# Kernel tuning notes

Measured on AMD Instinct MI355X. Metric: run time of the kernel, lower is better.

The kernel has to match this reference:

```python
import jax, jax.numpy as jnp
import numpy as np

N = 100000      # nodes
E = 800000      # edges
IN1 = 128       # gcn input feature dim
IN2 = 64        # lstm input feature dim
H = 128         # hidden_channels
B = 32          # lstm batch
T = 200         # lstm seq len
OUT = 1         # out_channels
TARGET = jnp.array([0, 1000, 2000, 3000, 4000, 5000, 6000, 7000])  # numgcnE=8


def setup_inputs() -> dict:
    key = jax.random.key(0)
    ks = jax.random.split(key, 20)
    s = 0.05
    inp = {
        "data0": jax.random.normal(ks[0], (B, T, IN2), jnp.float32),
        "data1": jax.random.normal(ks[1], (N, IN1), jnp.float32),
        "edge_index": jax.random.randint(ks[2], (2, E), 0, N, dtype=jnp.int64),
        # GCNConv layers (weight stored [in, out])
        "W1": jax.random.normal(ks[3], (IN1, H), jnp.float32) * s,
        "b1": jnp.zeros((H,), jnp.float32),
        "W2": jax.random.normal(ks[4], (H, H), jnp.float32) * s,
        "b2": jnp.zeros((H,), jnp.float32),
        # LSTM1 (gate order i,f,g,o as in torch)
        "Wih1": jax.random.normal(ks[5], (4 * H, IN2), jnp.float32) * s,
        "Whh1": jax.random.normal(ks[6], (4 * H, H), jnp.float32) * s,
        "bih1": jnp.zeros((4 * H,), jnp.float32),
        "bhh1": jnp.zeros((4 * H,), jnp.float32),
        # LSTM2
        "Wih2": jax.random.normal(ks[7], (4 * H, H), jnp.float32) * s,
        "Whh2": jax.random.normal(ks[8], (4 * H, H), jnp.float32) * s,
        "bih2": jnp.zeros((4 * H,), jnp.float32),
        "bhh2": jnp.zeros((4 * H,), jnp.float32),
        # MLP head: (numgcnE+1)*H -> (numgcnE+1)*H/2 -> OUT
        "m1_w": jax.random.normal(ks[9], (9 * H, 9 * H // 2), jnp.float32) * s,
        "m1_b": jnp.zeros((9 * H // 2,), jnp.float32),
        "m2_w": jax.random.normal(ks[10], (9 * H // 2, OUT), jnp.float32) * s,
        "m2_b": jnp.zeros((OUT,), jnp.float32),
    }
    return inp


def gcn_conv(x, W, b, src, dst, n):
    # PyG GCNConv: self-loops + symmetric normalization, then scatter-add.
    xw = x @ W                                                     # [N, H]
    ones = jnp.ones(src.shape[0], xw.dtype)
    deg = jax.ops.segment_sum(ones, dst, num_segments=n) + 1.0     # +1 self-loop
    dinv = jax.lax.rsqrt(deg)                                      # [N]
    norm = dinv[src] * dinv[dst]                                   # [E]
    agg = jax.ops.segment_sum(xw[src] * norm[:, None], dst, num_segments=n)
    agg = agg + xw * (dinv * dinv)[:, None]                        # self-loop msgs
    return agg + b


def lstm_final(x_tbi, Wih, Whh, bih, bhh):
    # x_tbi: [T, Bsz, in]; returns final hidden state h_T [Bsz, H]
    Bsz = x_tbi.shape[1]
    Hh = Whh.shape[1]
    bias = bih + bhh

    def step(carry, xt):
        h, c = carry
        g = xt @ Wih.T + h @ Whh.T + bias                          # [Bsz, 4H]
        i, f, gg, o = jnp.split(g, 4, axis=-1)
        c = jax.nn.sigmoid(f) * c + jax.nn.sigmoid(i) * jnp.tanh(gg)
        h = jax.nn.sigmoid(o) * jnp.tanh(c)
        return (h, c), None

    init = (jnp.zeros((Bsz, Hh), x_tbi.dtype), jnp.zeros((Bsz, Hh), x_tbi.dtype))
    (h, c), _ = jax.lax.scan(step, init, x_tbi)
    return h


def reference(data0, data1, edge_index, W1, b1, W2, b2,
              Wih1, Whh1, bih1, bhh1, Wih2, Whh2, bih2, bhh2,
              m1_w, m1_b, m2_w, m2_b):
    src, dst = edge_index[0], edge_index[1]
    n = data1.shape[0]
    # two GCN layers with ReLU
    h = jax.nn.relu(gcn_conv(data1, W1, b1, src, dst, n))
    h = jax.nn.relu(gcn_conv(h, W2, b2, src, dst, n))
    g = h[TARGET].reshape(-1)                                      # [numgcnE*H]
    # lstm1 over [B, T, IN2] (batch_first) -> final h_n [B, H]
    h1 = lstm_final(jnp.swapaxes(data0, 0, 1), Wih1, Whh1, bih1, bhh1)
    # lstm2 consumes h_n[None] as [batch=1, seq=B, H] -> final h [1, H]
    h2 = lstm_final(h1[:, None, :], Wih2, Whh2, bih2, bhh2)[0]     # [H]
    d = jnp.concatenate([g, h2])                                   # [(numgcnE+1)*H]
    return (d @ m1_w + m1_b) @ m2_w + m2_b                         # [OUT]
```

## Files before the change

### kernel.cpp

```cpp
#include <hip/hip_runtime.h>
#include <hip/hip_bf16.h>
#include <cstring>

using bf16 = __hip_bfloat16;
typedef _Float16 h2v __attribute__((ext_vector_type(2)));
typedef _Float16 h8v __attribute__((ext_vector_type(8)));

#if __has_builtin(__builtin_amdgcn_fdot2)
__device__ __forceinline__ float FDOT2(h2v a, h2v b, float c) {
    return __builtin_amdgcn_fdot2(a, b, c, false);
}
#else
__device__ __forceinline__ float FDOT2(h2v a, h2v b, float c) {
    return c + (float)a.x * (float)b.x + (float)a.y * (float)b.y;
}
#endif

__device__ __forceinline__ float sigm_f(float x) {
    return __builtin_amdgcn_rcpf(1.f + __expf(-x));
}
__device__ __forceinline__ float tanh_f(float x) {
    return 1.f - 2.f * __builtin_amdgcn_rcpf(1.f + __expf(2.f * x));
}

constexpr int NH    = 128;
constexpr int G4    = 512;
constexpr int TSEQ  = 200;
constexpr int BBATCH= 32;
constexpr int NTGT  = 8;

constexpr int LCAP1 = 1024;
constexpr int S1CAP = LCAP1 + NTGT;
constexpr int LCAP2 = 8192;
constexpr int S2CAP = LCAP2 + S1CAP;

constexpr size_t algn(size_t x) { return (x + 255) & ~size_t(255); }
constexpr size_t OFF_GX1  = 0;
constexpr size_t OFF_GX2  = algn(OFF_GX1  + 6400ull * G4 * 4);
constexpr size_t OFF_DEG  = algn(OFF_GX2  + 32ull * G4 * 4);
constexpr size_t OFF_DINV = algn(OFF_DEG  + 100000ull * 4);
constexpr size_t OFF_SL1  = algn(OFF_DINV + 100000ull * 4);
constexpr size_t OFF_SL2  = algn(OFF_SL1  + 100000ull * 4);
constexpr size_t OFF_CNT  = algn(OFF_SL2  + 100000ull * 4);
constexpr size_t OFF_L1   = algn(OFF_CNT  + 64);
constexpr size_t OFF_S1   = algn(OFF_L1   + (size_t)LCAP1 * 8);
constexpr size_t OFF_L2   = algn(OFF_S1   + (size_t)S1CAP * 4);
constexpr size_t OFF_S2   = algn(OFF_L2   + (size_t)LCAP2 * 8);
constexpr size_t OFF_XW1  = algn(OFF_S2   + (size_t)S2CAP * 4);
constexpr size_t OFF_H1   = algn(OFF_XW1  + (size_t)S2CAP * NH * 4);
constexpr size_t OFF_XW2  = algn(OFF_H1   + (size_t)S1CAP * NH * 4);
constexpr size_t OFF_DVEC = algn(OFF_XW2  + (size_t)S1CAP * NH * 4);
constexpr size_t OFF_H1F  = algn(OFF_DVEC + 1152ull * 4);
constexpr size_t OFF_CACC = algn(OFF_H1F  + 32ull * NH * 4);
constexpr size_t WS_NEEDED = OFF_CACC + 576ull * 4;

__device__ __forceinline__ int edge_at(const int* ei, int E, int is64, int row, int e) {
    return is64 ? ei[(((size_t)row * E) + e) * 2] : ei[((size_t)row * E) + e];
}

__device__ __forceinline__ float dinv_of(const int* deg, int v) {
    return rsqrtf((float)deg[v] + 1.0f);
}

__global__ void k_canary(unsigned int* out, unsigned int bits) {
    if (threadIdx.x == 0) out[0] = bits;
}


__global__ void k_init(const int* ei, int* deg, int* slot1, int* slot2, int* cnt,
                       float* colacc, int n) {
    int i = blockIdx.x * 256 + threadIdx.x;
    if (i < 14) cnt[i] = 0;
    if (i == 15) cnt[15] = (ei[1] == 0 && ei[3] == 0 && ei[5] == 0 && ei[7] == 0) ? 1 : 0;
    if (i < 576) colacc[i] = 0.f;
    for (; i < n; i += gridDim.x * 256) { deg[i] = 0; slot1[i] = -1; slot2[i] = -1; }
}

__global__ void k_deg_l1(const int* ei, int E, int* deg, int2* l1, int* cnt) {
    int is64 = cnt[15];
    for (int e = blockIdx.x * 256 + threadIdx.x; e < E; e += gridDim.x * 256) {
        int d = edge_at(ei, E, is64, 1, e);
        if ((unsigned)d < 100000u) atomicAdd(&deg[d], 1);
        if (d <= 7000 && d >= 0 && d % 1000 == 0) {
            int s = edge_at(ei, E, is64, 0, e);
            int idx = atomicAdd(&cnt[0], 1);
            if (idx < LCAP1) l1[idx] = make_int2(s, d);
        }
    }
}

__global__ void k_s1(const int2* l1, int* cnt, int* slot1, int* s1list,
                     int* slot2, int* s2list) {
    __shared__ int ns1;
    if (threadIdx.x == 0) ns1 = 0;
    __syncthreads();
    int m = min(cnt[0], LCAP1);
    for (int i = threadIdx.x; i < NTGT + m; i += blockDim.x) {
        int v = (i < NTGT) ? i * 1000 : l1[i - NTGT].x;
        if ((unsigned)v >= 100000u) continue;
        int old = atomicCAS(&slot1[v], -1, -2);
        if (old == -1) {
            int idx = atomicAdd(&ns1, 1);
            if (idx < S1CAP) { s1list[idx] = v; atomicExch(&slot1[v], idx); }
        }
    }
    __syncthreads();
    int n1 = min(ns1, S1CAP);
    if (threadIdx.x == 0) cnt[1] = n1;
    for (int i = threadIdx.x; i < n1; i += blockDim.x) {
        int v = s1list[i];
        int old = atomicCAS(&slot2[v], -1, -2);
        if (old == -1) {
            int idx = atomicAdd(&cnt[2], 1);
            if (idx < S2CAP) { s2list[idx] = v; atomicExch(&slot2[v], idx); }
        }
    }
}

__global__ void k_l2(const int* ei, int E, const int* slot1,
                     int2* l2, int* cnt, int* slot2, int* s2list) {
    int is64 = cnt[15];
    for (int e = blockIdx.x * 256 + threadIdx.x; e < E; e += gridDim.x * 256) {
        int d = edge_at(ei, E, is64, 1, e);
        if ((unsigned)d >= 100000u) continue;
        if (slot1[d] >= 0) {
            int s = edge_at(ei, E, is64, 0, e);
            if ((unsigned)s >= 100000u) continue;
            int idx = atomicAdd(&cnt[3], 1);
            if (idx < LCAP2) l2[idx] = make_int2(s, d);
            int old = atomicCAS(&slot2[s], -1, -2);
            if (old == -1) {
                int j = atomicAdd(&cnt[2], 1);
                if (j < S2CAP) { s2list[j] = s; atomicExch(&slot2[s], j); }
            }
        }
    }
}


__global__ void k_xw1(const float* x, const float* W, const int* s2list, const int* cnt, float* xw1) {
    int i = blockIdx.x;
    if (i >= min(cnt[2], S2CAP)) return;
    int node = s2list[i];
    __shared__ float xs[NH];
    int c = threadIdx.x;
    xs[c] = x[(size_t)node * NH + c];
    __syncthreads();
    float acc = 0.f;
    #pragma unroll 8
    for (int k = 0; k < NH; k++) acc += xs[k] * W[(size_t)k * NH + c];
    xw1[(size_t)i * NH + c] = acc;
}

__global__ void k_h1init(const float* xw1, const int* s1list, const int* cnt,
                         const int* slot2, const int* deg, float* h1) {
    int i = blockIdx.x;
    if (i >= min(cnt[1], S1CAP)) return;
    int node = s1list[i];
    int s2 = slot2[node];
    if (s2 < 0 || s2 >= S2CAP) s2 = 0;
    float v = dinv_of(deg, node);
    h1[i * NH + threadIdx.x] = xw1[(size_t)s2 * NH + threadIdx.x] * v * v;
}

__global__ void k_h1scat(const float* xw1, const int2* l2, const int* cnt,
                         const int* slot1, const int* slot2, const int* deg, float* h1) {
    int e = blockIdx.x;
    if (e >= min(cnt[3], LCAP2)) return;
    int2 sd = l2[e];
    int t1 = slot1[sd.y], s2 = slot2[sd.x];
    if (t1 < 0 || t1 >= S1CAP || s2 < 0 || s2 >= S2CAP) return;
    float w = dinv_of(deg, sd.x) * dinv_of(deg, sd.y);
    atomicAdd(&h1[t1 * NH + threadIdx.x],
              xw1[(size_t)s2 * NH + threadIdx.x] * w);
}

__global__ void k_xw2(const float* h1, const float* W, const float* b1, const int* cnt, float* xw2) {
    int i = blockIdx.x;
    if (i >= min(cnt[1], S1CAP)) return;
    __shared__ float xs[NH];
    int c = threadIdx.x;
    xs[c] = fmaxf(h1[i * NH + c] + b1[c], 0.f);
    __syncthreads();
    float acc = 0.f;
    #pragma unroll 8
    for (int k = 0; k < NH; k++) acc += xs[k] * W[(size_t)k * NH + c];
    xw2[(size_t)i * NH + c] = acc;
}

__global__ void k_gout(const float* xw2, const int2* l1, const int* cnt,
                       const int* slot1, const int* deg, const float* b2, float* dvec) {
    int t = blockIdx.x;
    int tgt = t * 1000;
    int c = threadIdx.x;
    float vt = dinv_of(deg, tgt);
    int st = slot1[tgt]; if (st < 0 || st >= S1CAP) st = 0;
    float acc = xw2[(size_t)st * NH + c] * vt * vt;
    int m = min(cnt[0], LCAP1);
    for (int e = 0; e < m; e++) {
        int2 sd = l1[e];
        if (sd.y == tgt) {
            int ss = slot1[sd.x];
            if (ss >= 0 && ss < S1CAP)
                acc += xw2[(size_t)ss * NH + c] * dinv_of(deg, sd.x) * vt;
        }
    }
    acc += b2[c];
    dvec[t * NH + c] = fmaxf(acc, 0.f);
}


__global__ __launch_bounds__(256) void k_gx1(const float* data0, const float* Wih,
                                             const float* bih, const float* bhh, float* gx) {
    constexpr int LDP = 68;
    __shared__ float As[64 * LDP];
    __shared__ float Bs[64 * LDP];
    int tid = threadIdx.x;
    int rb = blockIdx.x >> 3;
    int gb = blockIdx.x & 7;
    int r0 = rb * 64, g0 = gb * 64;
    for (int i = tid; i < 64 * 64; i += 256) {
        int rr = i >> 6, k = i & 63;
        int r = r0 + rr, b = r & 31, t = r >> 5;
        As[rr * LDP + k] = data0[((size_t)b * TSEQ + t) * 64 + k];
        Bs[rr * LDP + k] = Wih[(size_t)(g0 + rr) * 64 + k];
    }
    __syncthreads();
    int tr = (tid & 15) * 4;
    int tg = (tid >> 4) * 4;
    float acc[4][4] = {};
    #pragma unroll
    for (int k4 = 0; k4 < 16; k4++) {
        float4 a0 = *(const float4*)&As[(tr + 0) * LDP + k4 * 4];
        float4 a1 = *(const float4*)&As[(tr + 1) * LDP + k4 * 4];
        float4 a2 = *(const float4*)&As[(tr + 2) * LDP + k4 * 4];
        float4 a3 = *(const float4*)&As[(tr + 3) * LDP + k4 * 4];
        float4 b0 = *(const float4*)&Bs[(tg + 0) * LDP + k4 * 4];
        float4 b1 = *(const float4*)&Bs[(tg + 1) * LDP + k4 * 4];
        float4 b2 = *(const float4*)&Bs[(tg + 2) * LDP + k4 * 4];
        float4 b3 = *(const float4*)&Bs[(tg + 3) * LDP + k4 * 4];
        const float4 av[4] = {a0, a1, a2, a3};
        const float4 bv[4] = {b0, b1, b2, b3};
        #pragma unroll
        for (int i = 0; i < 4; i++)
            #pragma unroll
            for (int j = 0; j < 4; j++)
                acc[i][j] += av[i].x * bv[j].x + av[i].y * bv[j].y
                           + av[i].z * bv[j].z + av[i].w * bv[j].w;
    }
    float bias[4];
    #pragma unroll
    for (int j = 0; j < 4; j++) bias[j] = bih[g0 + tg + j] + bhh[g0 + tg + j];
    #pragma unroll
    for (int i = 0; i < 4; i++) {
        size_t row = (size_t)(r0 + tr + i) * G4 + g0 + tg;
        #pragma unroll
        for (int j = 0; j < 4; j++) gx[row + j] = acc[i][j] + bias[j];
    }
}

__global__ void k_gx2(const float* h1f, const float* Wih,
                      const float* bih, const float* bhh, float* gx) {
    int t = blockIdx.x;
    __shared__ float xs[NH];
    int tid = threadIdx.x;
    int g0 = tid, g1 = tid + 256;
    if (tid < NH) xs[tid] = h1f[t * NH + tid];
    __syncthreads();
    float a0 = bih[g0] + bhh[g0];
    float a1 = bih[g1] + bhh[g1];
    #pragma unroll 4
    for (int k = 0; k < NH; k++) {
        a0 += Wih[(size_t)g0 * NH + k] * xs[k];
        a1 += Wih[(size_t)g1 * NH + k] * xs[k];
    }
    gx[(size_t)t * G4 + g0] = a0;
    gx[(size_t)t * G4 + g1] = a1;
}

template<int T, int NB>
__global__ __launch_bounds__(256, 1) void k_lstm(const float* gx, const float* Whh, float* hfinal) {
    int b = blockIdx.x;
    int tid = threadIdx.x;
    int w = tid >> 6, l = tid & 63;
    int j = w * 32 + (l & 31);
    int role = l >> 5;
    int r0 = role ? (j + NH) : j;
    int r1 = role ? (j + 3 * NH) : (j + 2 * NH);
    __shared__ __align__(16) _Float16 hbuf[2][NH];
    h2v w0[NH / 2], w1[NH / 2];
    #pragma unroll
    for (int k = 0; k < NH; k += 4) {
        float4 a = *(const float4*)&Whh[(size_t)r0 * NH + k];
        w0[k / 2]     = h2v{(_Float16)a.x, (_Float16)a.y};
        w0[k / 2 + 1] = h2v{(_Float16)a.z, (_Float16)a.w};
        float4 c4 = *(const float4*)&Whh[(size_t)r1 * NH + k];
        w1[k / 2]     = h2v{(_Float16)c4.x, (_Float16)c4.y};
        w1[k / 2 + 1] = h2v{(_Float16)c4.z, (_Float16)c4.w};
    }
    if (tid < NH) { hbuf[0][tid] = (_Float16)0.f; hbuf[1][tid] = (_Float16)0.f; }
    float c = 0.f, hout = 0.f;
    float nx0 = gx[((size_t)0 * NB + b) * G4 + r0];
    float nx1 = gx[((size_t)0 * NB + b) * G4 + r1];
    __syncthreads();
    for (int t = 0; t < T; t++) {
        const h8v* hv8 = (const h8v*)hbuf[t & 1];
        float a0 = nx0, a1 = nx1;
        int tn = (t + 1 < T) ? (t + 1) : t;
        nx0 = gx[((size_t)tn * NB + b) * G4 + r0];
        nx1 = gx[((size_t)tn * NB + b) * G4 + r1];
        float p0 = 0.f, q0 = 0.f, p1 = 0.f, q1 = 0.f;
        #pragma unroll
        for (int m = 0; m < NH / 8; m++) {
            h8v h8 = hv8[m];
            h2v ha = __builtin_shufflevector(h8, h8, 0, 1);
            h2v hb = __builtin_shufflevector(h8, h8, 2, 3);
            h2v hc = __builtin_shufflevector(h8, h8, 4, 5);
            h2v hd = __builtin_shufflevector(h8, h8, 6, 7);
            p0 = FDOT2(w0[4 * m],     ha, p0);
            q0 = FDOT2(w0[4 * m + 1], hb, q0);
            p0 = FDOT2(w0[4 * m + 2], hc, p0);
            q0 = FDOT2(w0[4 * m + 3], hd, q0);
            p1 = FDOT2(w1[4 * m],     ha, p1);
            q1 = FDOT2(w1[4 * m + 1], hb, q1);
            p1 = FDOT2(w1[4 * m + 2], hc, p1);
            q1 = FDOT2(w1[4 * m + 3], hd, q1);
        }
        float ga = a0 + p0 + q0;
        float gb = a1 + p1 + q1;
        float s  = sigm_f(ga);
        float tg = role ? sigm_f(gb) : tanh_f(gb);
        float u  = s * tg;
        float fv = __shfl_xor(s,  32);
        float ov = __shfl_xor(tg, 32);
        if (role == 0) {
            c = fv * c + u;
            hout = ov * tanh_f(c);
            hbuf[(t + 1) & 1][j] = (_Float16)hout;
        }
        __syncthreads();
    }
    if (role == 0) hfinal[(size_t)b * NH + j] = hout;
}

__global__ __launch_bounds__(64) void k_head1(const float* dvec, const float* m1w, float* colacc) {
    int rg = blockIdx.x & 7;
    int cg = blockIdx.x >> 3;
    int col = cg * 64 + threadIdx.x;
    int r0 = rg * 144;
    float acc = 0.f;
    #pragma unroll 4
    for (int i = r0; i < r0 + 144; i++)
        acc += dvec[i] * m1w[(size_t)i * 576 + col];
    atomicAdd(&colacc[col], acc);
}

__global__ __launch_bounds__(256) void k_head2(const float* colacc, const float* m1b,
                                               const float* m2w, const float* m2b,
                                               unsigned int* out) {
    __shared__ float wr[4];
    int j = threadIdx.x;
    float sum = 0.f;
    for (int col = j; col < 576; col += 256)
        sum += (colacc[col] + m1b[col]) * m2w[col];
    #pragma unroll
    for (int off = 32; off > 0; off >>= 1) sum += __shfl_down(sum, off, 64);
    if ((j & 63) == 0) wr[j >> 6] = sum;
    __syncthreads();
    if (j == 0) {
        float s = wr[0] + wr[1] + wr[2] + wr[3] + m2b[0];
        bf16 hb = __float2bfloat16(s);
        unsigned short u;
        memcpy(&u, &hb, 2);
        out[0] = ((unsigned int)u << 16) | u;
    }
}


extern "C" void kernel_launch(void* const* d_in, const int* in_sizes, int n_in,
                              void* d_out, int out_size, void* d_ws, size_t ws_size,
                              hipStream_t stream) {
    const float* data0 = (const float*)d_in[0];
    const float* data1 = (const float*)d_in[1];
    const int*   ei    = (const int*)d_in[2];
    const float* W1    = (const float*)d_in[3];
    const float* b1    = (const float*)d_in[4];
    const float* W2    = (const float*)d_in[5];
    const float* b2    = (const float*)d_in[6];
    const float* Wih1  = (const float*)d_in[7];
    const float* Whh1  = (const float*)d_in[8];
    const float* bih1  = (const float*)d_in[9];
    const float* bhh1  = (const float*)d_in[10];
    const float* Wih2  = (const float*)d_in[11];
    const float* Whh2  = (const float*)d_in[12];
    const float* bih2  = (const float*)d_in[13];
    const float* bhh2  = (const float*)d_in[14];
    const float* m1w   = (const float*)d_in[15];
    const float* m1b   = (const float*)d_in[16];
    const float* m2w   = (const float*)d_in[17];
    const float* m2b   = (const float*)d_in[18];

    const int n = in_sizes[1] / NH;
    const int E = in_sizes[2] / 2;

    char* ws = (char*)d_ws;
    float* gx1   = (float*)(ws + OFF_GX1);
    float* gx2   = (float*)(ws + OFF_GX2);
    int*   deg   = (int*)  (ws + OFF_DEG);
    int*   slot1 = (int*)  (ws + OFF_SL1);
    int*   slot2 = (int*)  (ws + OFF_SL2);
    int*   cnt   = (int*)  (ws + OFF_CNT);
    int2*  l1    = (int2*) (ws + OFF_L1);
    int*   s1l   = (int*)  (ws + OFF_S1);
    int2*  l2    = (int2*) (ws + OFF_L2);
    int*   s2l   = (int*)  (ws + OFF_S2);
    float* xw1   = (float*)(ws + OFF_XW1);
    float* h1    = (float*)(ws + OFF_H1);
    float* xw2   = (float*)(ws + OFF_XW2);
    float* dvec  = (float*)(ws + OFF_DVEC);
    float* h1f   = (float*)(ws + OFF_H1F);
    float* cacc  = (float*)(ws + OFF_CACC);

    float v = 1.0f + (ws_size < WS_NEEDED ? 1.0f : 0.0f) + (n_in != 19 ? 2.0f : 0.0f);
    unsigned int fb; memcpy(&fb, &v, 4);
    unsigned int hi = fb >> 16;
    unsigned int canary_bits = (hi << 16) | hi;
    k_canary <<<1, 64, 0, stream>>>((unsigned int*)d_out, canary_bits);

    int nb = (n + 255) / 256;
    int eb = (E + 255) / 256;

    k_init   <<<nb, 256, 0, stream>>>(ei, deg, slot1, slot2, cnt, cacc, n);
    k_deg_l1 <<<eb, 256, 0, stream>>>(ei, E, deg, l1, cnt);
    k_s1     <<<1, 256, 0, stream>>>(l1, cnt, slot1, s1l, slot2, s2l);
    k_l2     <<<eb, 256, 0, stream>>>(ei, E, slot1, l2, cnt, slot2, s2l);
    k_xw1    <<<S2CAP, NH, 0, stream>>>(data1, W1, s2l, cnt, xw1);
    k_h1init <<<S1CAP, NH, 0, stream>>>(xw1, s1l, cnt, slot2, deg, h1);
    k_h1scat <<<LCAP2, NH, 0, stream>>>(xw1, l2, cnt, slot1, slot2, deg, h1);
    k_xw2    <<<S1CAP, NH, 0, stream>>>(h1, W2, b1, cnt, xw2);
    k_gout   <<<NTGT, NH, 0, stream>>>(xw2, l1, cnt, slot1, deg, b2, dvec);
    k_gx1    <<<800, 256, 0, stream>>>(data0, Wih1, bih1, bhh1, gx1);
    k_lstm<TSEQ, BBATCH><<<BBATCH, 256, 0, stream>>>(gx1, Whh1, h1f);
    k_gx2    <<<BBATCH, 256, 0, stream>>>(h1f, Wih2, bih2, bhh2, gx2);
    k_lstm<BBATCH, 1>  <<<1, 256, 0, stream>>>(gx2, Whh2, dvec + 1024);
    k_head1  <<<72, 64, 0, stream>>>(dvec, m1w, cacc);
    k_head2  <<<1, 256, 0, stream>>>(cacc, m1b, m2w, m2b, (unsigned int*)d_out);
    (void)out_size;
}
```

Before: 408.9 us.

## Fuse dependent kernels with last-block-done completion pattern to cut launches

Merges several small kernel pairs (degree scan with seed-set build, xw2 with target aggregation, head1 with head2) using a global atomic counter so the last finishing block performs the dependent tail work. The self-loop term is folded into the scatter as an explicit (v,v) edge, and h1 zeroing plus the canary write move into the init kernel. This removes roughly five launches and their serialisation gaps. In exchange, the tail work runs on a single block, and correctness relies on threadfence ordering.

```diff
diff --git a/kernel.cpp b/kernel.cpp
--- a/kernel.cpp
+++ b/kernel.cpp
@@ -62,21 +62,23 @@
     return rsqrtf((float)deg[v] + 1.0f);
 }
 
-__global__ void k_canary(unsigned int* out, unsigned int bits) {
-    if (threadIdx.x == 0) out[0] = bits;
-}
 
 
 __global__ void k_init(const int* ei, int* deg, int* slot1, int* slot2, int* cnt,
-                       float* colacc, int n) {
+                       float* colacc, float* h1, unsigned int* out, unsigned int bits, int n) {
     int i = blockIdx.x * 256 + threadIdx.x;
+    if (blockIdx.x == 0 && threadIdx.x == 0) out[0] = bits;
     if (i < 14) cnt[i] = 0;
     if (i == 15) cnt[15] = (ei[1] == 0 && ei[3] == 0 && ei[5] == 0 && ei[7] == 0) ? 1 : 0;
     if (i < 576) colacc[i] = 0.f;
+    for (int z = i; z < S1CAP * NH; z += gridDim.x * 256) h1[z] = 0.f;
     for (; i < n; i += gridDim.x * 256) { deg[i] = 0; slot1[i] = -1; slot2[i] = -1; }
 }
 
-__global__ void k_deg_l1(const int* ei, int E, int* deg, int2* l1, int* cnt) {
+
+__global__ __launch_bounds__(256) void k_scan1(const int* ei, int E, int* deg, int2* l1,
+                                               int* cnt, int* slot1, int* s1list,
+                                               int* slot2, int* s2list, int2* l2) {
     int is64 = cnt[15];
     for (int e = blockIdx.x * 256 + threadIdx.x; e < E; e += gridDim.x * 256) {
         int d = edge_at(ei, E, is64, 1, e);
@@ -87,38 +89,37 @@
             if (idx < LCAP1) l1[idx] = make_int2(s, d);
         }
     }
-}
-
-__global__ void k_s1(const int2* l1, int* cnt, int* slot1, int* s1list,
-                     int* slot2, int* s2list) {
-    __shared__ int ns1;
-    if (threadIdx.x == 0) ns1 = 0;
-    __syncthreads();
+    __threadfence();
+    __syncthreads();
+    __shared__ int lastf;
+    if (threadIdx.x == 0) lastf = (atomicAdd(&cnt[8], 1) == (int)gridDim.x - 1) ? 1 : 0;
+    __syncthreads();
+    if (!lastf) return;
+    __threadfence();
     int m = min(cnt[0], LCAP1);
-    for (int i = threadIdx.x; i < NTGT + m; i += blockDim.x) {
+    for (int i = threadIdx.x; i < NTGT + m; i += 256) {
         int v = (i < NTGT) ? i * 1000 : l1[i - NTGT].x;
         if ((unsigned)v >= 100000u) continue;
         int old = atomicCAS(&slot1[v], -1, -2);
         if (old == -1) {
-            int idx = atomicAdd(&ns1, 1);
-            if (idx < S1CAP) { s1list[idx] = v; atomicExch(&slot1[v], idx); }
+            int idx = atomicAdd(&cnt[1], 1);
+            if (idx < S1CAP) {
+                s1list[idx] = v; atomicExch(&slot1[v], idx);
+                int o2 = atomicCAS(&slot2[v], -1, -2);
+                if (o2 == -1) {
+                    int j2 = atomicAdd(&cnt[2], 1);
+                    if (j2 < S2CAP) { s2list[j2] = v; atomicExch(&slot2[v], j2); }
+                }
+                int se = atomicAdd(&cnt[3], 1);
+                if (se < LCAP2) l2[se] = make_int2(v, v);
+            }
         }
     }
-    __syncthreads();
-    int n1 = min(ns1, S1CAP);
-    if (threadIdx.x == 0) cnt[1] = n1;
-    for (int i = threadIdx.x; i < n1; i += blockDim.x) {
-        int v = s1list[i];
-        int old = atomicCAS(&slot2[v], -1, -2);
-        if (old == -1) {
-            int idx = atomicAdd(&cnt[2], 1);
-            if (idx < S2CAP) { s2list[idx] = v; atomicExch(&slot2[v], idx); }
-        }
-    }
-}
-
-__global__ void k_l2(const int* ei, int E, const int* slot1,
-                     int2* l2, int* cnt, int* slot2, int* s2list) {
+}
+
+
+__global__ __launch_bounds__(256) void k_l2(const int* ei, int E, const int* slot1,
+                                            int2* l2, int* cnt, int* slot2, int* s2list) {
     int is64 = cnt[15];
     for (int e = blockIdx.x * 256 + threadIdx.x; e < E; e += gridDim.x * 256) {
         int d = edge_at(ei, E, is64, 1, e);
@@ -152,17 +153,6 @@
     xw1[(size_t)i * NH + c] = acc;
 }
 
-__global__ void k_h1init(const float* xw1, const int* s1list, const int* cnt,
-                         const int* slot2, const int* deg, float* h1) {
-    int i = blockIdx.x;
-    if (i >= min(cnt[1], S1CAP)) return;
-    int node = s1list[i];
-    int s2 = slot2[node];
-    if (s2 < 0 || s2 >= S2CAP) s2 = 0;
-    float v = dinv_of(deg, node);
-    h1[i * NH + threadIdx.x] = xw1[(size_t)s2 * NH + threadIdx.x] * v * v;
-}
-
 __global__ void k_h1scat(const float* xw1, const int2* l2, const int* cnt,
                          const int* slot1, const int* slot2, const int* deg, float* h1) {
     int e = blockIdx.x;
@@ -175,38 +165,47 @@
               xw1[(size_t)s2 * NH + threadIdx.x] * w);
 }
 
-__global__ void k_xw2(const float* h1, const float* W, const float* b1, const int* cnt, float* xw2) {
+__global__ __launch_bounds__(128) void k_xw2g(const float* h1, const float* W, const float* b1,
+                                              int* cnt, const int2* l1, const int* slot1,
+                                              const int* deg, const float* b2,
+                                              float* xw2, float* dvec) {
     int i = blockIdx.x;
-    if (i >= min(cnt[1], S1CAP)) return;
-    __shared__ float xs[NH];
     int c = threadIdx.x;
-    xs[c] = fmaxf(h1[i * NH + c] + b1[c], 0.f);
-    __syncthreads();
-    float acc = 0.f;
-    #pragma unroll 8
-    for (int k = 0; k < NH; k++) acc += xs[k] * W[(size_t)k * NH + c];
-    xw2[(size_t)i * NH + c] = acc;
-}
-
-__global__ void k_gout(const float* xw2, const int2* l1, const int* cnt,
-                       const int* slot1, const int* deg, const float* b2, float* dvec) {
-    int t = blockIdx.x;
-    int tgt = t * 1000;
-    int c = threadIdx.x;
-    float vt = dinv_of(deg, tgt);
-    int st = slot1[tgt]; if (st < 0 || st >= S1CAP) st = 0;
-    float acc = xw2[(size_t)st * NH + c] * vt * vt;
+    if (i < min(cnt[1], S1CAP)) {
+        __shared__ float xs[NH];
+        xs[c] = fmaxf(h1[i * NH + c] + b1[c], 0.f);
+        __syncthreads();
+        float acc = 0.f;
+        #pragma unroll 8
+        for (int k = 0; k < NH; k++) acc += xs[k] * W[(size_t)k * NH + c];
+        xw2[(size_t)i * NH + c] = acc;
+    }
+    __threadfence();
+    __syncthreads();
+    __shared__ int lastf;
+    if (c == 0) lastf = (atomicAdd(&cnt[9], 1) == (int)gridDim.x - 1) ? 1 : 0;
+    __syncthreads();
+    if (!lastf) return;
+    __threadfence();
+    __shared__ float gacc[NTGT][NH];
+    #pragma unroll
+    for (int t = 0; t < NTGT; t++) gacc[t][c] = 0.f;
     int m = min(cnt[0], LCAP1);
     for (int e = 0; e < m; e++) {
         int2 sd = l1[e];
-        if (sd.y == tgt) {
-            int ss = slot1[sd.x];
-            if (ss >= 0 && ss < S1CAP)
-                acc += xw2[(size_t)ss * NH + c] * dinv_of(deg, sd.x) * vt;
-        }
-    }
-    acc += b2[c];
-    dvec[t * NH + c] = fmaxf(acc, 0.f);
+        int t = sd.y / 1000;
+        int ss = slot1[sd.x];
+        if (ss >= 0 && ss < S1CAP && t >= 0 && t < NTGT)
+            gacc[t][c] += xw2[(size_t)ss * NH + c] * dinv_of(deg, sd.x) * dinv_of(deg, sd.y);
+    }
+    #pragma unroll
+    for (int t = 0; t < NTGT; t++) {
+        int tgt = t * 1000;
+        float vt = dinv_of(deg, tgt);
+        int st = slot1[tgt]; if (st < 0 || st >= S1CAP) st = 0;
+        float a = gacc[t][c] + xw2[(size_t)st * NH + c] * vt * vt + b2[c];
+        dvec[t * NH + c] = fmaxf(a, 0.f);
+    }
 }
 
 
@@ -343,7 +342,10 @@
     if (role == 0) hfinal[(size_t)b * NH + j] = hout;
 }
 
-__global__ __launch_bounds__(64) void k_head1(const float* dvec, const float* m1w, float* colacc) {
+__global__ __launch_bounds__(64) void k_head(const float* dvec, const float* m1w,
+                                             float* colacc, const float* m1b,
+                                             const float* m2w, const float* m2b,
+                                             int* cnt, unsigned int* out) {
     int rg = blockIdx.x & 7;
     int cg = blockIdx.x >> 3;
     int col = cg * 64 + threadIdx.x;
@@ -353,22 +355,20 @@
     for (int i = r0; i < r0 + 144; i++)
         acc += dvec[i] * m1w[(size_t)i * 576 + col];
     atomicAdd(&colacc[col], acc);
-}
-
-__global__ __launch_bounds__(256) void k_head2(const float* colacc, const float* m1b,
-                                               const float* m2w, const float* m2b,
-                                               unsigned int* out) {
-    __shared__ float wr[4];
-    int j = threadIdx.x;
+    __threadfence();
+    __syncthreads();
+    __shared__ int lastf;
+    if (threadIdx.x == 0) lastf = (atomicAdd(&cnt[10], 1) == (int)gridDim.x - 1) ? 1 : 0;
+    __syncthreads();
+    if (!lastf) return;
+    __threadfence();
     float sum = 0.f;
-    for (int col = j; col < 576; col += 256)
-        sum += (colacc[col] + m1b[col]) * m2w[col];
+    for (int c2 = threadIdx.x; c2 < 576; c2 += 64)
+        sum += (colacc[c2] + m1b[c2]) * m2w[c2];
     #pragma unroll
     for (int off = 32; off > 0; off >>= 1) sum += __shfl_down(sum, off, 64);
-    if ((j & 63) == 0) wr[j >> 6] = sum;
-    __syncthreads();
-    if (j == 0) {
-        float s = wr[0] + wr[1] + wr[2] + wr[3] + m2b[0];
+    if (threadIdx.x == 0) {
+        float s = sum + m2b[0];
         bf16 hb = __float2bfloat16(s);
         unsigned short u;
         memcpy(&u, &hb, 2);
@@ -425,25 +425,21 @@
     unsigned int fb; memcpy(&fb, &v, 4);
     unsigned int hi = fb >> 16;
     unsigned int canary_bits = (hi << 16) | hi;
-    k_canary <<<1, 64, 0, stream>>>((unsigned int*)d_out, canary_bits);
 
     int nb = (n + 255) / 256;
     int eb = (E + 255) / 256;
 
-    k_init   <<<nb, 256, 0, stream>>>(ei, deg, slot1, slot2, cnt, cacc, n);
-    k_deg_l1 <<<eb, 256, 0, stream>>>(ei, E, deg, l1, cnt);
-    k_s1     <<<1, 256, 0, stream>>>(l1, cnt, slot1, s1l, slot2, s2l);
+    k_init   <<<nb, 256, 0, stream>>>(ei, deg, slot1, slot2, cnt, cacc, h1,
+                                      (unsigned int*)d_out, canary_bits, n);
+    k_scan1  <<<eb, 256, 0, stream>>>(ei, E, deg, l1, cnt, slot1, s1l, slot2, s2l, l2);
     k_l2     <<<eb, 256, 0, stream>>>(ei, E, slot1, l2, cnt, slot2, s2l);
     k_xw1    <<<S2CAP, NH, 0, stream>>>(data1, W1, s2l, cnt, xw1);
-    k_h1init <<<S1CAP, NH, 0, stream>>>(xw1, s1l, cnt, slot2, deg, h1);
     k_h1scat <<<LCAP2, NH, 0, stream>>>(xw1, l2, cnt, slot1, slot2, deg, h1);
-    k_xw2    <<<S1CAP, NH, 0, stream>>>(h1, W2, b1, cnt, xw2);
-    k_gout   <<<NTGT, NH, 0, stream>>>(xw2, l1, cnt, slot1, deg, b2, dvec);
+    k_xw2g   <<<S1CAP, NH, 0, stream>>>(h1, W2, b1, cnt, l1, slot1, deg, b2, xw2, dvec);
     k_gx1    <<<800, 256, 0, stream>>>(data0, Wih1, bih1, bhh1, gx1);
     k_lstm<TSEQ, BBATCH><<<BBATCH, 256, 0, stream>>>(gx1, Whh1, h1f);
     k_gx2    <<<BBATCH, 256, 0, stream>>>(h1f, Wih2, bih2, bhh2, gx2);
     k_lstm<BBATCH, 1>  <<<1, 256, 0, stream>>>(gx2, Whh2, dvec + 1024);
-    k_head1  <<<72, 64, 0, stream>>>(dvec, m1w, cacc);
-    k_head2  <<<1, 256, 0, stream>>>(cacc, m1b, m2w, m2b, (unsigned int*)d_out);
+    k_head   <<<72, 64, 0, stream>>>(dvec, m1w, cacc, m1b, m2w, m2b, cnt, (unsigned int*)d_out);
     (void)out_size;
 }
```

New measurement: 614.3 us. 1.5x slower.
